# Optimization experiments

Measured on AMD Instinct MI355X. Metric: run time of the kernel, lower is better.

## Reference

```python
import jax, jax.numpy as jnp
import numpy as np

EPS = 1e-5
N_CONV = 3
B = 2048  # number of crystals


def _bn_eval(x, gamma, beta):
    # Eval-mode BatchNorm with running_mean=0, running_var=1.
    return x * (gamma / jnp.sqrt(1.0 + EPS)) + beta


def _conv_layer(atom_fea, nbr_fea, nbr_fea_idx, W, b, g1, b1, g2, b2):
    # Canonical CGCNN ConvLayer.
    N, M = nbr_fea_idx.shape
    F = atom_fea.shape[1]
    nbr_atom = atom_fea[nbr_fea_idx]                                  # [N,M,F]
    self_atom = jnp.broadcast_to(atom_fea[:, None, :], (N, M, F))     # [N,M,F]
    total = jnp.concatenate([self_atom, nbr_atom, nbr_fea], axis=2)   # [N,M,2F+nbr]
    gated = total @ W + b                                             # [N,M,2F]
    gated = _bn_eval(gated, g1, b1)
    flt, core = jnp.split(gated, 2, axis=2)
    nbr_sumed = jnp.sum(jax.nn.sigmoid(flt) * jax.nn.softplus(core), axis=1)  # [N,F]
    nbr_sumed = _bn_eval(nbr_sumed, g2, b2)
    return jax.nn.softplus(atom_fea + nbr_sumed)


def setup_inputs() -> dict:
    key = jax.random.key(0)
    ks = jax.random.split(key, 24)
    N, M = 60000, 12
    OA, NB, F, OE, E, H = 92, 41, 64, 8, 16, 128
    s = 0.05
    inp = {
        "atom_fea": jax.random.normal(ks[0], (N, OA), jnp.float32),
        "nbr_fea": jax.random.normal(ks[1], (N, M, NB), jnp.float32),
        "nbr_fea_idx": jax.random.randint(ks[2], (N, M), 0, N),
        "segment_ids": jnp.sort(jax.random.randint(ks[3], (N,), 0, B)),
        "extra_fea": jax.random.normal(ks[4], (B, OE), jnp.float32),
        # embedding_atom
        "W_embed": jax.random.normal(ks[5], (OA, F), jnp.float32) * s,
        "b_embed": jnp.zeros((F,), jnp.float32),
        # conv layers (stacked over n_conv=3)
        "conv_W": jax.random.normal(ks[6], (N_CONV, 2 * F + NB, 2 * F), jnp.float32) * s,
        "conv_b": jnp.zeros((N_CONV, 2 * F), jnp.float32),
        "bn1_g": jnp.ones((N_CONV, 2 * F), jnp.float32),
        "bn1_b": jnp.zeros((N_CONV, 2 * F), jnp.float32),
        "bn2_g": jnp.ones((N_CONV, F), jnp.float32),
        "bn2_b": jnp.zeros((N_CONV, F), jnp.float32),
        # embedding_extra
        "W_extra": jax.random.normal(ks[7], (OE, E), jnp.float32) * s,
        "b_extra": jnp.zeros((E,), jnp.float32),
        "bnx_g": jnp.ones((E,), jnp.float32),
        "bnx_b": jnp.zeros((E,), jnp.float32),
        # conv_to_fc
        "W_fc": jax.random.normal(ks[8], (F + E, H), jnp.float32) * s,
        "b_fc": jnp.zeros((H,), jnp.float32),
        "W_out0": jax.random.normal(ks[9], (H, 1), jnp.float32) * s,
        "b_out0": jnp.zeros((1,), jnp.float32),
        "W_out1": jax.random.normal(ks[10], (H, 2), jnp.float32) * s,
        "b_out1": jnp.zeros((2,), jnp.float32),
        "W_out2": jax.random.normal(ks[11], (H, 1), jnp.float32) * s,
        "b_out2": jnp.zeros((1,), jnp.float32),
    }
    return inp


def reference(atom_fea, nbr_fea, nbr_fea_idx, segment_ids, extra_fea,
              W_embed, b_embed, conv_W, conv_b, bn1_g, bn1_b, bn2_g, bn2_b,
              W_extra, b_extra, bnx_g, bnx_b, W_fc, b_fc,
              W_out0, b_out0, W_out1, b_out1, W_out2, b_out2):
    x = atom_fea @ W_embed + b_embed                                  # [N,F]
    extra = jax.nn.softplus(_bn_eval(extra_fea @ W_extra + b_extra, bnx_g, bnx_b))  # [B,E]
    for i in range(N_CONV):
        x = _conv_layer(x, nbr_fea, nbr_fea_idx, conv_W[i], conv_b[i],
                        bn1_g[i], bn1_b[i], bn2_g[i], bn2_b[i])
    # segment-mean pooling (replaces per-crystal python loop)
    sums = jax.ops.segment_sum(x, segment_ids, num_segments=B)        # [B,F]
    cnts = jax.ops.segment_sum(jnp.ones((x.shape[0],), x.dtype), segment_ids, num_segments=B)
    crys = sums / jnp.maximum(cnts, 1.0)[:, None]
    crys = jnp.concatenate([crys, extra], axis=1)                     # [B,F+E]
    crys = jax.nn.softplus(crys @ W_fc + b_fc)                        # [B,H]
    out0 = crys @ W_out0 + b_out0
    out1 = jax.nn.log_softmax(crys @ W_out1 + b_out1, axis=1)         # classification [B,2]
    out2 = crys @ W_out2 + b_out2
    return out0, out1, out2
```

## Files before the change

### kernel.cpp

```cpp
#include <hip/hip_runtime.h>
#include <math.h>
#include <stdint.h>

#define N_ATOMS 60000
#define M_NBR   12
#define NBF     41
#define B_CRYS  2048
#define EPSBN   1e-5f
#define GA      8
#define ROWS    (GA * M_NBR)
#define GRID_F  (N_ATOMS / GA)
#define WIMG_L  24576

typedef __attribute__((ext_vector_type(8))) short bf8;
typedef __attribute__((ext_vector_type(4))) float f32x4;
#define MFMA_B16(a, b, c) __builtin_amdgcn_mfma_f32_16x16x32_bf16(a, b, c, 0, 0, 0)

__device__ __forceinline__ short f2bf(float f) {
  uint32_t u = __builtin_bit_cast(uint32_t, f);
  u += 0x7FFFu + ((u >> 16) & 1u);
  return (short)(u >> 16);
}
__device__ __forceinline__ float lo16(uint32_t u) {
  return __builtin_bit_cast(float, u << 16);
}
__device__ __forceinline__ float hi16(uint32_t u) {
  return __builtin_bit_cast(float, u & 0xFFFF0000u);
}
__device__ __forceinline__ float sp(float x) {
  return (x > 15.f) ? x : __logf(1.f + __expf(x));
}
__device__ __forceinline__ float sig(float x) {
  return 1.f / (1.f + __expf(-x));
}

__global__ __launch_bounds__(256) void k_wprep(
    const float* __restrict__ conv_W, const float* __restrict__ bn1_g,
    unsigned short* __restrict__ Wimg) {
  const int gid = blockIdx.x * 256 + threadIdx.x;
  if (gid >= 3 * WIMG_L) return;
  const int layer = gid / WIMG_L, rem = gid % WIMG_L;
  const int which = rem / 8192, r2 = rem % 8192;
  const int frag = r2 >> 9, lane = (r2 >> 3) & 63, j = r2 & 7;
  const int ct = frag >> 1, ks = frag & 1;
  const int quad = lane >> 4, l15 = lane & 15;
  const int jc = ct * 16 + l15;
  const int oc = (jc & 1) ? (jc >> 1) + 64 : (jc >> 1);
  const float s = bn1_g[layer * 128 + oc] * rsqrtf(1.f + EPSBN);
  const int k = ks * 32 + quad * 8 + j;
  const float* Wc = conv_W + (size_t)layer * 169 * 128;
  float v = 0.f;
  if (which == 0) {
    if (k < NBF) v = Wc[(128 + k) * 128 + oc] * s;
  } else if (which == 1) {
    v = Wc[k * 128 + oc] * s;
  } else {
    v = Wc[(64 + k) * 128 + oc] * s;
  }
  Wimg[gid] = (unsigned short)f2bf(v);
}

__global__ __launch_bounds__(256) void k_embed2(
    const float* __restrict__ A, const float* __restrict__ W,
    const float* __restrict__ bias, float* __restrict__ X,
    unsigned int* __restrict__ XbU) {
  const int lane = threadIdx.x & 63, wv = threadIdx.x >> 6;
  const int quad = lane >> 4, l15 = lane & 15;
  const int gw = blockIdx.x * 4 + wv, nw = gridDim.x * 4;
  bf8 Bf[3][4];
  float bs[4];
#pragma unroll
  for (int ct = 0; ct < 4; ++ct) {
    const int col = ct * 16 + l15;
    bs[ct] = bias[col];
#pragma unroll
    for (int ks = 0; ks < 3; ++ks) {
      bf8 b;
#pragma unroll
      for (int i = 0; i < 8; ++i) {
        const int k = ks * 32 + quad * 8 + i;
        b[i] = (k < 92) ? f2bf(W[k * 64 + col]) : (short)0;
      }
      Bf[ks][ct] = b;
    }
  }
  for (int rt = gw; rt < 3750; rt += nw) {
    const int rbase = rt * 16;
    const float* ar = A + (size_t)(rbase + l15) * 92;
    const float4 p0 = *(const float4*)(ar + quad * 8);
    const float4 p1 = *(const float4*)(ar + quad * 8 + 4);
    const float4 p2 = *(const float4*)(ar + 32 + quad * 8);
    const float4 p3 = *(const float4*)(ar + 32 + quad * 8 + 4);
    bf8 A0, A1, A2;
    A0[0] = f2bf(p0.x); A0[1] = f2bf(p0.y); A0[2] = f2bf(p0.z); A0[3] = f2bf(p0.w);
    A0[4] = f2bf(p1.x); A0[5] = f2bf(p1.y); A0[6] = f2bf(p1.z); A0[7] = f2bf(p1.w);
    A1[0] = f2bf(p2.x); A1[1] = f2bf(p2.y); A1[2] = f2bf(p2.z); A1[3] = f2bf(p2.w);
    A1[4] = f2bf(p3.x); A1[5] = f2bf(p3.y); A1[6] = f2bf(p3.z); A1[7] = f2bf(p3.w);
#pragma unroll
    for (int i = 0; i < 8; ++i) {
      const int k = 64 + quad * 8 + i;
      A2[i] = (k < 92) ? f2bf(ar[k]) : (short)0;
    }
    const f32x4 z = {0.f, 0.f, 0.f, 0.f};
    f32x4 acc[4];
#pragma unroll
    for (int ct = 0; ct < 4; ++ct) {
      acc[ct] = MFMA_B16(A0, Bf[0][ct], z);
      acc[ct] = MFMA_B16(A1, Bf[1][ct], acc[ct]);
      acc[ct] = MFMA_B16(A2, Bf[2][ct], acc[ct]);
    }
#pragma unroll
    for (int ct = 0; ct < 4; ++ct)
#pragma unroll
      for (int r = 0; r < 4; ++r) {
        const int row = rbase + quad * 4 + r;
        const float v = acc[ct][r] + bs[ct];
        X[(size_t)row * 64 + ct * 16 + l15] = v;
        const unsigned int u = (unsigned short)f2bf(v);
        const unsigned int p = __shfl_xor((int)u, 1);
        if (!(l15 & 1))
          XbU[(size_t)row * 32 + ct * 8 + (l15 >> 1)] = u | (p << 16);
      }
  }
}

__global__ __launch_bounds__(256) void k_ygemm3(
    const unsigned short* __restrict__ Xb,
    const unsigned short* __restrict__ WiS, const float* __restrict__ bc,
    const float* __restrict__ g1, const float* __restrict__ b1,
    unsigned int* __restrict__ Ysu) {
  const int lane = threadIdx.x & 63, wv = threadIdx.x >> 6;
  const int quad = lane >> 4, l15 = lane & 15;
  const int gw = blockIdx.x * 4 + wv, nw = gridDim.x * 4;
  const float inv = rsqrtf(1.f + EPSBN);
  bf8 Bf[2][8];
  float bs[8];
#pragma unroll
  for (int ct = 0; ct < 8; ++ct) {
    const int j = ct * 16 + l15;
    const int oc = (j & 1) ? (j >> 1) + 64 : (j >> 1);
    bs[ct] = bc[oc] * (g1[oc] * inv) + b1[oc];
#pragma unroll
    for (int ks = 0; ks < 2; ++ks)
      Bf[ks][ct] = *(const bf8*)(WiS + ((ct * 2 + ks) * 64 + lane) * 8);
  }
  for (int rt = gw; rt < 3750; rt += nw) {
    const int rbase = rt * 16;
    const unsigned short* xr = Xb + (size_t)(rbase + l15) * 64;
    const bf8 A0 = *(const bf8*)(xr + quad * 8);
    const bf8 A1 = *(const bf8*)(xr + 32 + quad * 8);
    const f32x4 z = {0.f, 0.f, 0.f, 0.f};
#pragma unroll
    for (int ct = 0; ct < 8; ++ct) {
      f32x4 acc = MFMA_B16(A0, Bf[0][ct], z);
      acc = MFMA_B16(A1, Bf[1][ct], acc);
#pragma unroll
      for (int r = 0; r < 4; ++r) {
        const unsigned int u = (unsigned short)f2bf(acc[r] + bs[ct]);
        const unsigned int p = __shfl_xor((int)u, 1);
        if (!(l15 & 1))
          Ysu[(size_t)(rbase + quad * 4 + r) * 64 + ct * 8 + (l15 >> 1)] =
              u | (p << 16);
      }
    }
  }
}

__global__ __launch_bounds__(256, 5) void k_fused3(
    float* __restrict__ X, const unsigned short* __restrict__ XbIn,
    unsigned int* __restrict__ XbOutU, const unsigned int* __restrict__ Ysu,
    const float* __restrict__ NF, const int* __restrict__ IDX,
    const unsigned short* __restrict__ Wi, const float* __restrict__ g2,
    const float* __restrict__ b2) {
  __shared__ __align__(16) unsigned int eb32[ROWS * 64];
  unsigned short* eb16 = (unsigned short*)eb32;
  float* stage = (float*)eb32;
  const int tid = threadIdx.x;
  const int lane = tid & 63, wv = tid >> 6;
  const int quad = lane >> 4, l15 = lane & 15;
  const int g = blockIdx.x;
  const int ntile = (wv < 2) ? 2 : 1;

  bf8 Ax0[2], Ax1[2];
#pragma unroll
  for (int ti = 0; ti < 2; ++ti) {
    if (ti < ntile) {
      const int rbase = (wv + ti * 4) * 16;
      const int jr = IDX[g * ROWS + rbase + l15];
      const unsigned short* xr = XbIn + (size_t)jr * 64 + quad * 8;
      Ax0[ti] = *(const bf8*)xr;
      Ax1[ti] = *(const bf8*)(xr + 32);
    }
  }

  const float4* s4 = (const float4*)(NF + (size_t)g * (ROWS * NBF));
#pragma unroll
  for (int it = 0; it < 4; ++it) {
    const int w = tid + it * 256;
    if (w < (ROWS * NBF) / 4) ((float4*)stage)[w] = s4[w];
  }
  __syncthreads();

  bf8 Ae0[2], Ae1[2];
#pragma unroll
  for (int ti = 0; ti < 2; ++ti) {
    if (ti < ntile) {
      const int rbase = (wv + ti * 4) * 16;
      const float* rp = stage + (rbase + l15) * NBF;
      bf8 a0, a1;
#pragma unroll
      for (int i = 0; i < 8; ++i) a0[i] = f2bf(rp[quad * 8 + i]);
      if (quad == 0) {
#pragma unroll
        for (int i = 0; i < 8; ++i) a1[i] = f2bf(rp[32 + i]);
      } else if (quad == 1) {
        a1[0] = f2bf(rp[40]);
#pragma unroll
        for (int i = 1; i < 8; ++i) a1[i] = 0;
      } else {
#pragma unroll
        for (int i = 0; i < 8; ++i) a1[i] = 0;
      }
      Ae0[ti] = a0;
      Ae1[ti] = a1;
    }
  }
  __syncthreads();

#pragma unroll
  for (int ti = 0; ti < 2; ++ti) {
    if (ti < ntile) {
      const int rbase = (wv + ti * 4) * 16;
      const f32x4 z = {0.f, 0.f, 0.f, 0.f};
#pragma unroll 1
      for (int ct = 0; ct < 8; ++ct) {
        const bf8 Be0 = *(const bf8*)(Wi + ((ct * 2 + 0) * 64 + lane) * 8);
        const bf8 Be1 = *(const bf8*)(Wi + ((ct * 2 + 1) * 64 + lane) * 8);
        const bf8 Bn0 =
            *(const bf8*)(Wi + 16384 + ((ct * 2 + 0) * 64 + lane) * 8);
        const bf8 Bn1 =
            *(const bf8*)(Wi + 16384 + ((ct * 2 + 1) * 64 + lane) * 8);
        f32x4 acc = MFMA_B16(Ax0[ti], Bn0, z);
        acc = MFMA_B16(Ax1[ti], Bn1, acc);
        acc = MFMA_B16(Ae0[ti], Be0, acc);
        acc = MFMA_B16(Ae1[ti], Be1, acc);
        const int j = ct * 16 + l15;
        const int c = j >> 1, h = j & 1;
#pragma unroll
        for (int r = 0; r < 4; ++r) {
          const int row = rbase + quad * 4 + r;
          eb16[row * 128 + ((c + row) & 63) * 2 + h] =
              (unsigned short)f2bf(acc[r]);
        }
      }
    }
  }
  __syncthreads();

  const float inv = rsqrtf(1.f + EPSBN);
  const float s2 = g2[lane] * inv, o2 = b2[lane];
#pragma unroll
  for (int al = 0; al < 2; ++al) {
    const int a_local = wv * 2 + al;
    const int n = g * GA + a_local;
    const uint32_t ys = Ysu[(size_t)n * 64 + lane];
    const float ysf = lo16(ys), ysc = hi16(ys);
    float acc = 0.f;
#pragma unroll
    for (int m = 0; m < 12; ++m) {
      const int row = a_local * 12 + m;
      const uint32_t eu = eb32[row * 64 + ((lane + row) & 63)];
      acc += sig(ysf + lo16(eu)) * sp(ysc + hi16(eu));
    }
    const size_t o = (size_t)n * 64 + lane;
    const float res = sp(X[o] + acc * s2 + o2);
    X[o] = res;
    const unsigned int u = (unsigned short)f2bf(res);
    const unsigned int p = __shfl_xor((int)u, 1);
    if (!(lane & 1)) XbOutU[(size_t)n * 32 + (lane >> 1)] = u | (p << 16);
  }
}

__device__ __forceinline__ int lbound(const int* __restrict__ a, int n, int v) {
  int lo = 0, hi = n;
  while (lo < hi) {
    int mid = (lo + hi) >> 1;
    if (a[mid] < v) lo = mid + 1; else hi = mid;
  }
  return lo;
}

__global__ __launch_bounds__(128) void k_head(
    const float* __restrict__ Xf, const int* __restrict__ seg,
    const float* __restrict__ EF, const float* __restrict__ Wx,
    const float* __restrict__ bx, const float* __restrict__ gx,
    const float* __restrict__ bxb, const float* __restrict__ Wfc,
    const float* __restrict__ bfc, const float* __restrict__ Wo0,
    const float* __restrict__ bo0, const float* __restrict__ Wo1,
    const float* __restrict__ bo1, const float* __restrict__ Wo2,
    const float* __restrict__ bo2, float* __restrict__ out) {
  const int b = blockIdx.x;
  const int t = threadIdx.x;
  __shared__ float vbuf[80];
  __shared__ float part[128];
  __shared__ float4 r4[128];
  const int lo = lbound(seg, N_ATOMS, b);
  const int hi = lbound(seg, N_ATOMS, b + 1);
  const int col = t & 63, half = t >> 6;
  float s = 0.f;
  for (int r = lo + half; r < hi; r += 2) s += Xf[(size_t)r * 64 + col];
  part[t] = s;
  __syncthreads();
  if (t < 64) {
    vbuf[t] = (part[t] + part[t + 64]) / fmaxf((float)(hi - lo), 1.f);
  } else if (t < 80) {
    const int e = t - 64;
    float a = bx[e];
#pragma unroll
    for (int k = 0; k < 8; ++k) a += EF[b * 8 + k] * Wx[k * 16 + e];
    a = a * (gx[e] * rsqrtf(1.f + EPSBN)) + bxb[e];
    vbuf[t] = sp(a);
  }
  __syncthreads();
  float h = bfc[t];
#pragma unroll
  for (int k = 0; k < 80; ++k) h += vbuf[k] * Wfc[k * 128 + t];
  h = sp(h);
  r4[t] = make_float4(h * Wo0[t], h * Wo1[2 * t], h * Wo1[2 * t + 1],
                      h * Wo2[t]);
  __syncthreads();
  for (int st2 = 64; st2 > 0; st2 >>= 1) {
    if (t < st2) {
      float4 a = r4[t], c = r4[t + st2];
      r4[t] = make_float4(a.x + c.x, a.y + c.y, a.z + c.z, a.w + c.w);
    }
    __syncthreads();
  }
  if (t == 0) {
    float4 r = r4[0];
    out[b] = r.x + bo0[0];
    float z0 = r.y + bo1[0], z1 = r.z + bo1[1];
    float mx = fmaxf(z0, z1);
    float lse = mx + __logf(__expf(z0 - mx) + __expf(z1 - mx));
    out[B_CRYS + 2 * b] = z0 - lse;
    out[B_CRYS + 2 * b + 1] = z1 - lse;
    out[3 * B_CRYS + b] = r.w + bo2[0];
  }
}

extern "C" void kernel_launch(void* const* d_in, const int* in_sizes, int n_in,
                              void* d_out, int out_size, void* d_ws,
                              size_t ws_size, hipStream_t stream) {
  const float* atom_fea = (const float*)d_in[0];
  const float* nbr_fea  = (const float*)d_in[1];
  const int*   nbr_idx  = (const int*)d_in[2];
  const int*   seg      = (const int*)d_in[3];
  const float* extra    = (const float*)d_in[4];
  const float* W_embed  = (const float*)d_in[5];
  const float* b_embed  = (const float*)d_in[6];
  const float* conv_W   = (const float*)d_in[7];
  const float* conv_b   = (const float*)d_in[8];
  const float* bn1_g    = (const float*)d_in[9];
  const float* bn1_b    = (const float*)d_in[10];
  const float* bn2_g    = (const float*)d_in[11];
  const float* bn2_b    = (const float*)d_in[12];
  const float* W_extra  = (const float*)d_in[13];
  const float* b_extra  = (const float*)d_in[14];
  const float* bnx_g    = (const float*)d_in[15];
  const float* bnx_b    = (const float*)d_in[16];
  const float* W_fc     = (const float*)d_in[17];
  const float* b_fc     = (const float*)d_in[18];
  const float* W_out0   = (const float*)d_in[19];
  const float* b_out0   = (const float*)d_in[20];
  const float* W_out1   = (const float*)d_in[21];
  const float* b_out1   = (const float*)d_in[22];
  const float* W_out2   = (const float*)d_in[23];
  const float* b_out2   = (const float*)d_in[24];
  float* out = (float*)d_out;

  float* x = (float*)d_ws;
  unsigned int* xbu0 = (unsigned int*)(x + (size_t)N_ATOMS * 64);
  unsigned int* xbu1 = xbu0 + (size_t)N_ATOMS * 32;
  unsigned int* ysu = xbu1 + (size_t)N_ATOMS * 32;
  unsigned short* Wimg = (unsigned short*)(ysu + (size_t)N_ATOMS * 64);

  hipLaunchKernelGGL(k_wprep, dim3((3 * WIMG_L) / 256), dim3(256), 0, stream,
                     conv_W, bn1_g, Wimg);
  hipLaunchKernelGGL(k_embed2, dim3(256), dim3(256), 0, stream, atom_fea,
                     W_embed, b_embed, x, xbu0);
  unsigned int* xin = xbu0;
  unsigned int* xout = xbu1;
  for (int i = 0; i < 3; ++i) {
    hipLaunchKernelGGL(k_ygemm3, dim3(256), dim3(256), 0, stream,
                       (const unsigned short*)xin,
                       Wimg + (size_t)i * WIMG_L + 8192, conv_b + i * 128,
                       bn1_g + i * 128, bn1_b + i * 128, ysu);
    hipLaunchKernelGGL(k_fused3, dim3(GRID_F), dim3(256), 0, stream, x,
                       (const unsigned short*)xin, xout,
                       (const unsigned int*)ysu, nbr_fea, nbr_idx,
                       Wimg + (size_t)i * WIMG_L, bn2_g + i * 64,
                       bn2_b + i * 64);
    unsigned int* tmp = xin;
    xin = xout;
    xout = tmp;
  }
  hipLaunchKernelGGL(k_head, dim3(B_CRYS), dim3(128), 0, stream, x, seg, extra,
                     W_extra, b_extra, bnx_g, bnx_b, W_fc, b_fc, W_out0, b_out0,
                     W_out1, b_out1, W_out2, b_out2, out);
}
```

Measured before the change: 570.0 us.

## Fuse self-atom GEMM and bias into the per-neighbor conv kernel

Removes the separate k_ygemm3 launch that computed the self-atom projection plus folded bias into a Ysu buffer. The fused kernel now loads the self-atom bf16 rows and runs two extra MFMAs per column tile against the self-weight slice. The BN1-folded bias is carried as an extra weight row, matched by a constant 1.0 in the padded edge-feature column. This saves one launch and a write-and-read of the Ysu buffer per layer. In exchange the self-atom product is recomputed for each of the 12 neighbor rows, adding MFMA work and weight loads, and the bias is now rounded to bf16. The embed grid size also rises from 256 to 960 blocks.

```diff
diff --git a/kernel.cpp b/kernel.cpp
--- a/kernel.cpp
+++ b/kernel.cpp
@@ -35,7 +35,8 @@
 }
 
 __global__ __launch_bounds__(256) void k_wprep(
-    const float* __restrict__ conv_W, const float* __restrict__ bn1_g,
+    const float* __restrict__ conv_W, const float* __restrict__ conv_b,
+    const float* __restrict__ bn1_g, const float* __restrict__ bn1_b,
     unsigned short* __restrict__ Wimg) {
   const int gid = blockIdx.x * 256 + threadIdx.x;
   if (gid >= 3 * WIMG_L) return;
@@ -52,6 +53,7 @@
   float v = 0.f;
   if (which == 0) {
     if (k < NBF) v = Wc[(128 + k) * 128 + oc] * s;
+    else if (k == NBF) v = conv_b[layer * 128 + oc] * s + bn1_b[layer * 128 + oc];
   } else if (which == 1) {
     v = Wc[k * 128 + oc] * s;
   } else {
@@ -124,54 +126,11 @@
   }
 }
 
-__global__ __launch_bounds__(256) void k_ygemm3(
-    const unsigned short* __restrict__ Xb,
-    const unsigned short* __restrict__ WiS, const float* __restrict__ bc,
-    const float* __restrict__ g1, const float* __restrict__ b1,
-    unsigned int* __restrict__ Ysu) {
-  const int lane = threadIdx.x & 63, wv = threadIdx.x >> 6;
-  const int quad = lane >> 4, l15 = lane & 15;
-  const int gw = blockIdx.x * 4 + wv, nw = gridDim.x * 4;
-  const float inv = rsqrtf(1.f + EPSBN);
-  bf8 Bf[2][8];
-  float bs[8];
-#pragma unroll
-  for (int ct = 0; ct < 8; ++ct) {
-    const int j = ct * 16 + l15;
-    const int oc = (j & 1) ? (j >> 1) + 64 : (j >> 1);
-    bs[ct] = bc[oc] * (g1[oc] * inv) + b1[oc];
-#pragma unroll
-    for (int ks = 0; ks < 2; ++ks)
-      Bf[ks][ct] = *(const bf8*)(WiS + ((ct * 2 + ks) * 64 + lane) * 8);
-  }
-  for (int rt = gw; rt < 3750; rt += nw) {
-    const int rbase = rt * 16;
-    const unsigned short* xr = Xb + (size_t)(rbase + l15) * 64;
-    const bf8 A0 = *(const bf8*)(xr + quad * 8);
-    const bf8 A1 = *(const bf8*)(xr + 32 + quad * 8);
-    const f32x4 z = {0.f, 0.f, 0.f, 0.f};
-#pragma unroll
-    for (int ct = 0; ct < 8; ++ct) {
-      f32x4 acc = MFMA_B16(A0, Bf[0][ct], z);
-      acc = MFMA_B16(A1, Bf[1][ct], acc);
-#pragma unroll
-      for (int r = 0; r < 4; ++r) {
-        const unsigned int u = (unsigned short)f2bf(acc[r] + bs[ct]);
-        const unsigned int p = __shfl_xor((int)u, 1);
-        if (!(l15 & 1))
-          Ysu[(size_t)(rbase + quad * 4 + r) * 64 + ct * 8 + (l15 >> 1)] =
-              u | (p << 16);
-      }
-    }
-  }
-}
-
-__global__ __launch_bounds__(256, 5) void k_fused3(
+__global__ __launch_bounds__(256, 5) void k_fused4(
     float* __restrict__ X, const unsigned short* __restrict__ XbIn,
-    unsigned int* __restrict__ XbOutU, const unsigned int* __restrict__ Ysu,
-    const float* __restrict__ NF, const int* __restrict__ IDX,
-    const unsigned short* __restrict__ Wi, const float* __restrict__ g2,
-    const float* __restrict__ b2) {
+    unsigned int* __restrict__ XbOutU, const float* __restrict__ NF,
+    const int* __restrict__ IDX, const unsigned short* __restrict__ Wi,
+    const float* __restrict__ g2, const float* __restrict__ b2) {
   __shared__ __align__(16) unsigned int eb32[ROWS * 64];
   unsigned short* eb16 = (unsigned short*)eb32;
   float* stage = (float*)eb32;
@@ -181,7 +140,7 @@
   const int g = blockIdx.x;
   const int ntile = (wv < 2) ? 2 : 1;
 
-  bf8 Ax0[2], Ax1[2];
+  bf8 Ax0[2], Ax1[2], As0[2], As1[2];
 #pragma unroll
   for (int ti = 0; ti < 2; ++ti) {
     if (ti < ntile) {
@@ -190,6 +149,10 @@
       const unsigned short* xr = XbIn + (size_t)jr * 64 + quad * 8;
       Ax0[ti] = *(const bf8*)xr;
       Ax1[ti] = *(const bf8*)(xr + 32);
+      const int arow = g * GA + (rbase + l15) / M_NBR;
+      const unsigned short* sr = XbIn + (size_t)arow * 64 + quad * 8;
+      As0[ti] = *(const bf8*)sr;
+      As1[ti] = *(const bf8*)(sr + 32);
     }
   }
 
@@ -215,8 +178,9 @@
         for (int i = 0; i < 8; ++i) a1[i] = f2bf(rp[32 + i]);
       } else if (quad == 1) {
         a1[0] = f2bf(rp[40]);
-#pragma unroll
-        for (int i = 1; i < 8; ++i) a1[i] = 0;
+        a1[1] = (short)0x3F80;
+#pragma unroll
+        for (int i = 2; i < 8; ++i) a1[i] = 0;
       } else {
 #pragma unroll
         for (int i = 0; i < 8; ++i) a1[i] = 0;
@@ -236,12 +200,18 @@
       for (int ct = 0; ct < 8; ++ct) {
         const bf8 Be0 = *(const bf8*)(Wi + ((ct * 2 + 0) * 64 + lane) * 8);
         const bf8 Be1 = *(const bf8*)(Wi + ((ct * 2 + 1) * 64 + lane) * 8);
+        const bf8 Bs0 =
+            *(const bf8*)(Wi + 8192 + ((ct * 2 + 0) * 64 + lane) * 8);
+        const bf8 Bs1 =
+            *(const bf8*)(Wi + 8192 + ((ct * 2 + 1) * 64 + lane) * 8);
         const bf8 Bn0 =
             *(const bf8*)(Wi + 16384 + ((ct * 2 + 0) * 64 + lane) * 8);
         const bf8 Bn1 =
             *(const bf8*)(Wi + 16384 + ((ct * 2 + 1) * 64 + lane) * 8);
         f32x4 acc = MFMA_B16(Ax0[ti], Bn0, z);
         acc = MFMA_B16(Ax1[ti], Bn1, acc);
+        acc = MFMA_B16(As0[ti], Bs0, acc);
+        acc = MFMA_B16(As1[ti], Bs1, acc);
         acc = MFMA_B16(Ae0[ti], Be0, acc);
         acc = MFMA_B16(Ae1[ti], Be1, acc);
         const int j = ct * 16 + l15;
@@ -263,14 +233,12 @@
   for (int al = 0; al < 2; ++al) {
     const int a_local = wv * 2 + al;
     const int n = g * GA + a_local;
-    const uint32_t ys = Ysu[(size_t)n * 64 + lane];
-    const float ysf = lo16(ys), ysc = hi16(ys);
     float acc = 0.f;
 #pragma unroll
     for (int m = 0; m < 12; ++m) {
       const int row = a_local * 12 + m;
       const uint32_t eu = eb32[row * 64 + ((lane + row) & 63)];
-      acc += sig(ysf + lo16(eu)) * sp(ysc + hi16(eu));
+      acc += sig(lo16(eu)) * sp(hi16(eu));
     }
     const size_t o = (size_t)n * 64 + lane;
     const float res = sp(X[o] + acc * s2 + o2);
@@ -381,23 +349,17 @@
   float* x = (float*)d_ws;
   unsigned int* xbu0 = (unsigned int*)(x + (size_t)N_ATOMS * 64);
   unsigned int* xbu1 = xbu0 + (size_t)N_ATOMS * 32;
-  unsigned int* ysu = xbu1 + (size_t)N_ATOMS * 32;
-  unsigned short* Wimg = (unsigned short*)(ysu + (size_t)N_ATOMS * 64);
+  unsigned short* Wimg = (unsigned short*)(xbu1 + (size_t)N_ATOMS * 32);
 
   hipLaunchKernelGGL(k_wprep, dim3((3 * WIMG_L) / 256), dim3(256), 0, stream,
-                     conv_W, bn1_g, Wimg);
-  hipLaunchKernelGGL(k_embed2, dim3(256), dim3(256), 0, stream, atom_fea,
+                     conv_W, conv_b, bn1_g, bn1_b, Wimg);
+  hipLaunchKernelGGL(k_embed2, dim3(960), dim3(256), 0, stream, atom_fea,
                      W_embed, b_embed, x, xbu0);
   unsigned int* xin = xbu0;
   unsigned int* xout = xbu1;
   for (int i = 0; i < 3; ++i) {
-    hipLaunchKernelGGL(k_ygemm3, dim3(256), dim3(256), 0, stream,
-                       (const unsigned short*)xin,
-                       Wimg + (size_t)i * WIMG_L + 8192, conv_b + i * 128,
-                       bn1_g + i * 128, bn1_b + i * 128, ysu);
-    hipLaunchKernelGGL(k_fused3, dim3(GRID_F), dim3(256), 0, stream, x,
-                       (const unsigned short*)xin, xout,
-                       (const unsigned int*)ysu, nbr_fea, nbr_idx,
+    hipLaunchKernelGGL(k_fused4, dim3(GRID_F), dim3(256), 0, stream, x,
+                       (const unsigned short*)xin, xout, nbr_fea, nbr_idx,
                        Wimg + (size_t)i * WIMG_L, bn2_g + i * 64,
                        bn2_b + i * 64);
     unsigned int* tmp = xin;
```

After: 565.2 us. About the same (-0.9%).
